# Kernel tuning notes

Hardware: AMD Instinct MI355X
Metric: run time of the kernel (lower is better)

The kernel has to match this reference:

```python
import jax, jax.numpy as jnp
import numpy as np

TAU = 20.0   # membrane time constant (init kwarg tau)
TH = 1.0     # spike threshold (init kwarg threshold)
K = 10.0     # surrogate sigmoid sharpness

B, L = 131072, 400


def setup_inputs() -> dict:
    key = jax.random.key(0)
    I = jax.random.normal(key, (B, L), dtype=jnp.float32)
    return {"I": I}


def reference(I) -> jnp.ndarray:
    """LIF Euler integration over time with surrogate (straight-through) spikes.

    Faithful to the torch loop:
        v <- v + (-v/tau + I_t)
        s_soft = sigmoid(k*(v - th)); s_hard = (v >= th)
        s = stopgrad(s_hard - s_soft) + s_soft
        v <- v * (1 - stopgrad(s))
    Returns the spike raster [B, L]. (The original also returns a ragged
    Python list of per-sample spike latencies, which has data-dependent
    shape and is omitted from the jit-able reference.)
    """
    I_t = jnp.swapaxes(I, 0, 1)  # [L, B] for scan over time

    def step(v, It):
        v = v - v / TAU + It
        s_soft = jax.nn.sigmoid(K * (v - TH))
        s_hard = (v >= TH).astype(v.dtype)
        s = jax.lax.stop_gradient(s_hard - s_soft) + s_soft
        v = v * (1.0 - jax.lax.stop_gradient(s))
        return v, s

    v0 = jnp.zeros(I.shape[0], dtype=I.dtype)
    _, spikes_lb = jax.lax.scan(step, v0, I_t)  # [L, B]
    return jnp.swapaxes(spikes_lb, 0, 1)        # [B, L]
```

## Files before the change

### kernel.cpp

```cpp
#include <hip/hip_runtime.h>


typedef float f32x4 __attribute__((ext_vector_type(4)));

#define LIF_L 400

__global__ __launch_bounds__(256) void lif_kernel(const float* __restrict__ I,
                                                  float* __restrict__ out,
                                                  int nrows) {
    const int row = blockIdx.x * 256 + threadIdx.x;
    if (row >= nrows) return;

    const float* __restrict__ ib = I + (size_t)row * LIF_L;
    float*       __restrict__ ob = out + (size_t)row * LIF_L;

    constexpr int NC = 25;
    constexpr int D  = 5;
    constexpr int SD = 6;

    f32x4 ld[D][4];
    f32x4 sv[SD][4] = {};

    #pragma unroll
    for (int c = 0; c < D; ++c) {
        #pragma unroll
        for (int j = 0; j < 4; ++j)
            asm volatile("global_load_dwordx4 %0, %1, off offset:%c2"
                         : "=v"(ld[c][j])
                         : "v"(ib), "i"(c * 64 + j * 16));
    }

    constexpr int W[NC] = {16, 20, 24, 28, 32,
                           32, 32, 32, 32, 32, 32, 32, 32,
                           32, 32, 32, 32, 32, 32, 32, 32,
                           28, 24, 20, 16};

    constexpr float RCP = 0.05f;
    float v = 0.0f;

    #pragma unroll
    for (int c = 0; c < NC; ++c) {
        const int ls = c % D;
        const int ss = c % SD;

        asm volatile("s_waitcnt vmcnt(%c8)"
                     : "+v"(ld[ls][0]), "+v"(ld[ls][1]),
                       "+v"(ld[ls][2]), "+v"(ld[ls][3]),
                       "+v"(sv[ss][0]), "+v"(sv[ss][1]),
                       "+v"(sv[ss][2]), "+v"(sv[ss][3])
                     : "i"(W[c]));

        #pragma unroll
        for (int j = 0; j < 4; ++j) {
            const f32x4 x = ld[ls][j];
            f32x4 s;
            #pragma unroll
            for (int e = 0; e < 4; ++e) {
                const float p0 = v * RCP;
                const float er = __builtin_fmaf(-20.0f, p0, v);
                const float t  = __builtin_fmaf(er, RCP, p0);
                v = (v - t) + x[e];
                const bool sp = (v >= 1.0f);
                s[e] = sp ? 1.0f : 0.0f;
                v = sp ? 0.0f : v;
            }
            sv[ss][j] = s;
        }

        #pragma unroll
        for (int j = 0; j < 4; ++j)
            asm volatile("global_store_dwordx4 %0, %1, off offset:%c2"
                         :: "v"(ob), "v"(sv[ss][j]), "i"(c * 64 + j * 16)
                         : "memory");

        if (c + D < NC) {
            #pragma unroll
            for (int j = 0; j < 4; ++j)
                asm volatile("global_load_dwordx4 %0, %1, off offset:%c2"
                             : "=v"(ld[ls][j])
                             : "v"(ib), "i"((c + D) * 64 + j * 16));
        }
    }

    asm volatile("s_waitcnt vmcnt(0)"
                 : "+v"(sv[0][0]), "+v"(sv[0][1]), "+v"(sv[0][2]), "+v"(sv[0][3]),
                   "+v"(sv[1][0]), "+v"(sv[1][1]), "+v"(sv[1][2]), "+v"(sv[1][3]),
                   "+v"(sv[2][0]), "+v"(sv[2][1]), "+v"(sv[2][2]), "+v"(sv[2][3]),
                   "+v"(sv[3][0]), "+v"(sv[3][1]), "+v"(sv[3][2]), "+v"(sv[3][3]),
                   "+v"(sv[4][0]), "+v"(sv[4][1]), "+v"(sv[4][2]), "+v"(sv[4][3]),
                   "+v"(sv[5][0]), "+v"(sv[5][1]), "+v"(sv[5][2]), "+v"(sv[5][3]));
}

extern "C" void kernel_launch(void* const* d_in, const int* in_sizes, int n_in,
                              void* d_out, int out_size, void* d_ws, size_t ws_size,
                              hipStream_t stream) {
    const float* I = (const float*)d_in[0];
    float* out = (float*)d_out;
    const int nrows = in_sizes[0] / LIF_L;

    const int block = 256;
    const int grid = (nrows + block - 1) / block;
    lif_kernel<<<grid, block, 0, stream>>>(I, out, nrows);
}
```

Before: 436.0 us.

## Coalesce row loads and stores through swizzled LDS transpose staging

Instead of each thread loading and storing its own row with large strides, four threads cooperatively load 64-byte chunks of 64 rows into double-buffered shared memory with an XOR swizzle. Each thread then reads its row's chunk from LDS, computes spikes, and writes them to an LDS output buffer that is read back cooperatively and stored coalesced. The goal is better global memory coalescing for this bandwidth-bound kernel. The cost is two barriers per chunk, LDS traffic, a shallower prefetch depth, and removal of the tail bounds check, which assumes the row count is a multiple of 256.

```diff
diff --git a/kernel.cpp b/kernel.cpp
--- a/kernel.cpp
+++ b/kernel.cpp
@@ -6,89 +6,122 @@
 #define LIF_L 400
 
 __global__ __launch_bounds__(256) void lif_kernel(const float* __restrict__ I,
-                                                  float* __restrict__ out,
-                                                  int nrows) {
-    const int row = blockIdx.x * 256 + threadIdx.x;
-    if (row >= nrows) return;
+                                                  float* __restrict__ out) {
+    const int tid = threadIdx.x;
+    const int base_row = blockIdx.x * 256;
 
-    const float* __restrict__ ib = I + (size_t)row * LIF_L;
-    float*       __restrict__ ob = out + (size_t)row * LIF_L;
+    __shared__ f32x4 inb[2][256][4];
+    __shared__ f32x4 outb[256][4];
 
-    constexpr int NC = 25;
-    constexpr int D  = 5;
-    constexpr int SD = 6;
+    const int rr = tid >> 2;
+    const int p  = tid & 3;
+    const int pp = p ^ ((rr >> 1) & 3);
+    const int swt = (tid >> 1) & 3;
 
-    f32x4 ld[D][4];
-    f32x4 sv[SD][4] = {};
+    const float* ibp[4];
+    float* obp[4];
+    #pragma unroll
+    for (int i = 0; i < 4; ++i) {
+        const size_t r = (size_t)(base_row + rr + 64 * i);
+        ibp[i] = I   + r * LIF_L + p * 4;
+        obp[i] = out + r * LIF_L + p * 4;
+    }
+
+    f32x4 gl[2][4];
+    f32x4 so[2][4] = {};
 
     #pragma unroll
-    for (int c = 0; c < D; ++c) {
-        #pragma unroll
-        for (int j = 0; j < 4; ++j)
-            asm volatile("global_load_dwordx4 %0, %1, off offset:%c2"
-                         : "=v"(ld[c][j])
-                         : "v"(ib), "i"(c * 64 + j * 16));
-    }
+    for (int i = 0; i < 4; ++i)
+        asm volatile("global_load_dwordx4 %0, %1, off offset:0"
+                     : "=v"(gl[0][i]) : "v"(ibp[i]));
+    #pragma unroll
+    for (int i = 0; i < 4; ++i)
+        asm volatile("global_load_dwordx4 %0, %1, off offset:64"
+                     : "=v"(gl[1][i]) : "v"(ibp[i]));
+    asm volatile("s_waitcnt vmcnt(4)"
+                 : "+v"(gl[0][0]), "+v"(gl[0][1]), "+v"(gl[0][2]), "+v"(gl[0][3]));
+    #pragma unroll
+    for (int i = 0; i < 4; ++i)
+        inb[0][rr + 64 * i][pp] = gl[0][i];
+    #pragma unroll
+    for (int i = 0; i < 4; ++i)
+        asm volatile("global_load_dwordx4 %0, %1, off offset:128"
+                     : "=v"(gl[0][i]) : "v"(ibp[i]));
+    asm volatile("s_waitcnt lgkmcnt(0)\n\ts_barrier" ::: "memory");
 
-    constexpr int W[NC] = {16, 20, 24, 28, 32,
-                           32, 32, 32, 32, 32, 32, 32, 32,
-                           32, 32, 32, 32, 32, 32, 32, 32,
-                           28, 24, 20, 16};
+    constexpr int W[25] = {4, 8, 8, 8, 8, 8, 8, 8, 8, 8, 8, 8, 8,
+                           8, 8, 8, 8, 8, 8, 8, 8, 8, 8, 4, 4};
 
     constexpr float RCP = 0.05f;
     float v = 0.0f;
 
     #pragma unroll
-    for (int c = 0; c < NC; ++c) {
-        const int ls = c % D;
-        const int ss = c % SD;
+    for (int c = 0; c < 25; ++c) {
+        const int cb = c & 1;
+        const int nb = cb ^ 1;
 
-        asm volatile("s_waitcnt vmcnt(%c8)"
-                     : "+v"(ld[ls][0]), "+v"(ld[ls][1]),
-                       "+v"(ld[ls][2]), "+v"(ld[ls][3]),
-                       "+v"(sv[ss][0]), "+v"(sv[ss][1]),
-                       "+v"(sv[ss][2]), "+v"(sv[ss][3])
-                     : "i"(W[c]));
-
+        f32x4 xs[4], sp[4];
+        #pragma unroll
+        for (int j = 0; j < 4; ++j)
+            xs[j] = inb[cb][tid][j ^ swt];
         #pragma unroll
         for (int j = 0; j < 4; ++j) {
-            const f32x4 x = ld[ls][j];
-            f32x4 s;
             #pragma unroll
             for (int e = 0; e < 4; ++e) {
-                const float p0 = v * RCP;
-                const float er = __builtin_fmaf(-20.0f, p0, v);
-                const float t  = __builtin_fmaf(er, RCP, p0);
-                v = (v - t) + x[e];
-                const bool sp = (v >= 1.0f);
-                s[e] = sp ? 1.0f : 0.0f;
-                v = sp ? 0.0f : v;
+                const float q0 = v * RCP;
+                const float er = __builtin_fmaf(-20.0f, q0, v);
+                const float t  = __builtin_fmaf(er, RCP, q0);
+                v = (v - t) + xs[j][e];
+                const bool spk = (v >= 1.0f);
+                sp[j][e] = spk ? 1.0f : 0.0f;
+                v = spk ? 0.0f : v;
             }
-            sv[ss][j] = s;
         }
+
+        asm volatile("s_waitcnt lgkmcnt(0)\n\ts_barrier" ::: "memory");
 
         #pragma unroll
         for (int j = 0; j < 4; ++j)
-            asm volatile("global_store_dwordx4 %0, %1, off offset:%c2"
-                         :: "v"(ob), "v"(sv[ss][j]), "i"(c * 64 + j * 16)
-                         : "memory");
+            outb[tid][j ^ swt] = sp[j];
 
-        if (c + D < NC) {
+        if (c < 24) {
+            asm volatile("s_waitcnt vmcnt(%c8)"
+                         : "+v"(gl[nb][0]), "+v"(gl[nb][1]),
+                           "+v"(gl[nb][2]), "+v"(gl[nb][3]),
+                           "+v"(so[cb][0]), "+v"(so[cb][1]),
+                           "+v"(so[cb][2]), "+v"(so[cb][3])
+                         : "i"(W[c]));
             #pragma unroll
-            for (int j = 0; j < 4; ++j)
-                asm volatile("global_load_dwordx4 %0, %1, off offset:%c2"
-                             : "=v"(ld[ls][j])
-                             : "v"(ib), "i"((c + D) * 64 + j * 16));
+            for (int i = 0; i < 4; ++i)
+                inb[nb][rr + 64 * i][pp] = gl[nb][i];
+            if (c <= 21) {
+                #pragma unroll
+                for (int i = 0; i < 4; ++i)
+                    asm volatile("global_load_dwordx4 %0, %1, off offset:%c2"
+                                 : "=v"(gl[nb][i])
+                                 : "v"(ibp[i]), "i"((c + 3) * 64));
+            }
+        } else {
+            asm volatile("s_waitcnt vmcnt(4)"
+                         : "+v"(so[0][0]), "+v"(so[0][1]),
+                           "+v"(so[0][2]), "+v"(so[0][3]));
         }
+
+        asm volatile("s_waitcnt lgkmcnt(0)\n\ts_barrier" ::: "memory");
+
+        #pragma unroll
+        for (int i = 0; i < 4; ++i)
+            so[cb][i] = outb[rr + 64 * i][pp];
+        #pragma unroll
+        for (int i = 0; i < 4; ++i)
+            asm volatile("global_store_dwordx4 %1, %0, off offset:%c2"
+                         : "+v"(so[cb][i])
+                         : "v"(obp[i]), "i"(c * 64) : "memory");
     }
 
     asm volatile("s_waitcnt vmcnt(0)"
-                 : "+v"(sv[0][0]), "+v"(sv[0][1]), "+v"(sv[0][2]), "+v"(sv[0][3]),
-                   "+v"(sv[1][0]), "+v"(sv[1][1]), "+v"(sv[1][2]), "+v"(sv[1][3]),
-                   "+v"(sv[2][0]), "+v"(sv[2][1]), "+v"(sv[2][2]), "+v"(sv[2][3]),
-                   "+v"(sv[3][0]), "+v"(sv[3][1]), "+v"(sv[3][2]), "+v"(sv[3][3]),
-                   "+v"(sv[4][0]), "+v"(sv[4][1]), "+v"(sv[4][2]), "+v"(sv[4][3]),
-                   "+v"(sv[5][0]), "+v"(sv[5][1]), "+v"(sv[5][2]), "+v"(sv[5][3]));
+                 : "+v"(so[0][0]), "+v"(so[0][1]), "+v"(so[0][2]), "+v"(so[0][3]),
+                   "+v"(so[1][0]), "+v"(so[1][1]), "+v"(so[1][2]), "+v"(so[1][3]));
 }
 
 extern "C" void kernel_launch(void* const* d_in, const int* in_sizes, int n_in,
@@ -97,8 +130,7 @@
     const float* I = (const float*)d_in[0];
     float* out = (float*)d_out;
     const int nrows = in_sizes[0] / LIF_L;
+    const int grid = nrows / 256;
 
-    const int block = 256;
-    const int grid = (nrows + block - 1) / block;
-    lif_kernel<<<grid, block, 0, stream>>>(I, out, nrows);
+    lif_kernel<<<grid, 256, 0, stream>>>(I, out);
 }
```

Measured after the change: 395.7 us. 1.1x faster.
